# Performance work log

Measured on AMD Instinct MI355X. Metric: run time of the kernel, lower is better.

Reference implementation:

```python
import jax, jax.numpy as jnp
import numpy as np

BIG, SMALL = 13, 3
NK = 5                       # ceil(BIG / SMALL)
PADDING = SMALL - 1          # 2
EXTRA_PAD = PADDING - SMALL // 2   # 1
G = 2                        # group_in
C_OUT = 96
C_IN = G * C_OUT * NK        # 960
B, H, W = 16, 56, 56


def setup_inputs() -> dict:
    key = jax.random.key(0)
    k1, k2 = jax.random.split(key, 2)
    rng = np.random.default_rng(0)
    mid = BIG // 2
    real_pad = np.array([mid - i * SMALL - PADDING for i in range(NK)], dtype=np.int32)  # [4,1,-2,-5,-8]

    def perm_pads():
        # per output channel, a random permutation of the nk shift offsets
        return np.concatenate([rng.permutation(real_pad) for _ in range(C_OUT)])

    ph = np.stack([perm_pads() for _ in range(G)])  # (G, C_OUT*NK) horizontal shifts
    pv = np.stack([perm_pads() for _ in range(G)])  # (G, C_OUT*NK) vertical shifts
    pad_hv = np.concatenate([ph, pv], axis=0).T.astype(np.int32)  # (C_OUT*NK, 2*G)

    ids = []
    for _ in range(G):
        col = []
        for _ in range(C_OUT):
            arr = -np.ones(NK, dtype=np.int32)
            pos = rng.choice(NK, min(4, NK), replace=False)
            arr[pos] = np.arange(min(4, NK))
            col.append(arr)
        ids.append(np.concatenate(col))
    idx_identit = np.stack(ids).T.astype(np.int32)  # (C_OUT*NK, G)

    x = jax.random.normal(k1, (B, C_IN, H, W), jnp.float32)
    proj_w = jax.random.normal(k2, (C_OUT, C_IN), jnp.float32) * np.float32(1.0 / np.sqrt(C_IN))
    return {
        'x': x,
        'pad_hv': jnp.asarray(pad_hv),
        'idx_identit': jnp.asarray(idx_identit),
        'local_scale': jnp.ones((1, C_IN, 1, 1), jnp.float32),
        'local_bias': jnp.zeros((1, C_IN, 1, 1), jnp.float32),
        'proj_w': proj_w,
        'fuse_alpha': jnp.float32(0.7),
        'b': B, 'hout': H, 'wout': W,
    }


def reference(x, pad_hv, idx_identit, local_scale, local_bias, proj_w, fuse_alpha, b, hout, wout):
    p = EXTRA_PAD
    xp = jnp.pad(x, ((0, 0), (0, 0), (p, p), (p, p)), mode='edge')  # replicate pad
    Bx, Cin, Hp, Wp = xp.shape

    # per-channel shift offsets: channel ic = g*C_OUT*NK + slot, slot = co*NK + k
    ph = pad_hv[:, :G].T.reshape(-1)  # (C_IN,) horizontal (w-axis) shifts
    pv = pad_hv[:, G:].T.reshape(-1)  # (C_IN,) vertical (h-axis) shifts

    def gather_w(xc, s):  # xc: (B, Hp, Wp), s: scalar int shift
        idx = jnp.arange(wout) + p + s
        valid = ((idx >= 0) & (idx < Wp)).astype(xc.dtype)
        return xc[:, p:p + hout, jnp.clip(idx, 0, Wp - 1)] * valid[None, None, :]

    def gather_h(xc, s):
        idx = jnp.arange(hout) + p + s
        valid = ((idx >= 0) & (idx < Hp)).astype(xc.dtype)
        return xc[:, jnp.clip(idx, 0, Hp - 1), p:p + wout] * valid[None, :, None]

    xh = jax.vmap(gather_w, in_axes=(1, 0), out_axes=1)(xp, ph)  # (B, C_IN, hout, wout)
    xv = jax.vmap(gather_h, in_axes=(1, 0), out_axes=1)(xp, pv)
    x1 = xh.reshape(Bx, G, C_OUT, NK, hout, wout).sum((1, 3))    # horizontal-shift group
    x2 = xv.reshape(Bx, G, C_OUT, NK, hout, wout).sum((1, 3))    # vertical-shift group

    id_mask = (idx_identit.T.reshape(-1) >= 0).astype(xp.dtype)  # (C_IN,) identity slots
    x3 = (xp[:, :, p:p + hout, p:p + wout] * id_mask[None, :, None, None])
    x3 = x3.reshape(Bx, G, C_OUT, NK, hout, wout).sum((1, 3))    # identity group

    global_feat = (x1 + x2 + x3) / 3.0

    local = xp * (local_scale + 1e-5) + local_bias
    local = jax.image.resize(local, (Bx, Cin, hout, wout), method='bilinear')  # align_corners=False
    local = jnp.einsum('bchw,oc->bohw', local, proj_w)  # 1x1 conv, no bias

    return fuse_alpha * global_feat + (1.0 - fuse_alpha) * local
```

## Files before the change

### kernel.cpp

```cpp
#include <hip/hip_runtime.h>
#include <hip/hip_bf16.h>
#include <cstdint>
#include <cstddef>

#define B_    16
#define CIN   960
#define HH    56
#define WW_   56
#define GG    2
#define COUT  96
#define NK_   5
#define PIX   3136
#define NCH   30

#define WF_OFF   0
#define BIAS_OFF 46080
#define Y_OFF    46208

typedef __attribute__((ext_vector_type(8))) short bf16x8;
typedef __attribute__((ext_vector_type(4))) float f32x4;

__device__ __forceinline__ short f2b(float f) {
    union { float f; unsigned u; } c; c.f = f;
    unsigned r = (c.u + 0x7FFFu + ((c.u >> 16) & 1u)) >> 16;
    return (short)r;
}
__device__ __forceinline__ float b2f(short s) {
    union { unsigned u; float f; } c;
    c.u = ((unsigned)(unsigned short)s) << 16;
    return c.f;
}

#define GLOAD_LDS16(gp, lp)                                                        \
    __builtin_amdgcn_global_load_lds(                                              \
        (const __attribute__((address_space(1))) unsigned*)(gp),                   \
        (__attribute__((address_space(3))) unsigned*)(lp), 16, 0, 0)

#define WAITVM8() asm volatile("s_waitcnt vmcnt(8)" ::: "memory")
#define RBARRIER() asm volatile("s_barrier" ::: "memory")

__global__ void prep_wb(const float* __restrict__ pw, const float* __restrict__ sc,
                        short* __restrict__ wf) {
    int idx = blockIdx.x * 256 + threadIdx.x;
    if (idx >= NCH * 6 * 64) return;
    const int lane = idx & 63;
    const int nf   = idx >> 6;
    const int f    = nf % 6;
    const int n    = nf / 6;
    const int o    = f * 16 + (lane & 15);
    const int c0   = n * 32 + (lane >> 4) * 8;
    bf16x8 v;
#pragma unroll
    for (int k = 0; k < 8; ++k)
        v[k] = f2b(pw[o * CIN + c0 + k] * (sc[c0 + k] + 1e-5f));
    *(bf16x8*)(wf + (size_t)idx * 8) = v;
}

__global__ void prep_bias(const float* __restrict__ pw, const float* __restrict__ bi,
                          float* __restrict__ bias) {
    const int o = blockIdx.x;
    const int l = threadIdx.x;
    float s = 0.f;
    for (int c = l; c < CIN; c += 64) s += pw[o * CIN + c] * bi[c];
#pragma unroll
    for (int off = 32; off; off >>= 1) s += __shfl_down(s, off);
    if (l == 0) bias[o] = s;
}

__global__ __launch_bounds__(256)
void conv_mfma(const float* __restrict__ x, const short* __restrict__ wf,
               short* __restrict__ yb) {
    const int tid  = threadIdx.x;
    const int lane = tid & 63;
    const int wv   = tid >> 6;
    const int b    = blockIdx.y;
    const int px0  = blockIdx.x * 64;

    __shared__ __align__(16) char xs[3][8192];

    const float* xbase = x + (size_t)b * CIN * PIX + px0;

    const int pxl = wv * 16 + (lane & 15);
    const int kb  = lane >> 4;
    const int rbase = (pxl * 4) ^ (kb << 6);
    const short* const wfl = wf + lane * 8;

    f32x4 acc[6];
#pragma unroll
    for (int f = 0; f < 6; ++f) acc[f] = (f32x4){0.f, 0.f, 0.f, 0.f};

#define STAGE(bufp, c0)                                                          \
    {                                                                            \
        _Pragma("unroll")                                                        \
        for (int q = 0; q < 2; ++q) {                                            \
            const int i_  = wv * 2 + q;                                          \
            const int ch_ = (c0) + i_ * 4 + (lane >> 4);                         \
            const int px4 = (lane & 15) ^ (((i_ >> 1) & 3) << 2);                \
            GLOAD_LDS16(xbase + (size_t)ch_ * PIX + px4 * 4,                     \
                        (char*)(bufp) + i_ * 1024);                              \
        }                                                                        \
    }

#define WLOAD(dst, n2)                                                           \
    {                                                                            \
        _Pragma("unroll")                                                        \
        for (int f = 0; f < 6; ++f)                                              \
            dst[f] = *(const bf16x8*)(wfl + ((n2) * 6 + f) * 512);               \
    }

    bf16x8 afA[6], afB[6], afC[6];

    STAGE(xs[0], 0);
    STAGE(xs[1], 32);
    WLOAD(afA, 0);
    WLOAD(afB, 1);

#define STEP(n, BI, BS, CUR, NXT)                                                \
    {                                                                            \
        WAITVM8();                                                               \
        RBARRIER();                                                              \
        bf16x8 bfrag;                                                            \
        _Pragma("unroll")                                                        \
        for (int k = 0; k < 8; ++k)                                              \
            bfrag[k] = f2b(*(const float*)(xs[BI] + (kb * 8 + k) * 256 + rbase));\
        if ((n) + 2 < NCH) {                                                     \
            STAGE(xs[BS], ((n) + 2) * 32);                                       \
            WLOAD(NXT, (n) + 2);                                                 \
        }                                                                        \
        _Pragma("unroll")                                                        \
        for (int f = 0; f < 6; ++f)                                              \
            acc[f] = __builtin_amdgcn_mfma_f32_16x16x32_bf16(CUR[f], bfrag, acc[f], 0, 0, 0); \
    }

#pragma unroll 1
    for (int mm = 0; mm < 10; ++mm) {
        const int n0 = mm * 3;
        STEP(n0 + 0, 0, 2, afA, afC);
        STEP(n0 + 1, 1, 0, afB, afA);
        STEP(n0 + 2, 2, 1, afC, afB);
    }
#undef STEP
#undef WLOAD
#undef STAGE

    short* yp = yb + (size_t)b * COUT * PIX + px0 + pxl;
#pragma unroll
    for (int f = 0; f < 6; ++f) {
        const int o0 = f * 16 + (lane >> 4) * 4;
#pragma unroll
        for (int r = 0; r < 4; ++r)
            yp[(size_t)(o0 + r) * PIX] = f2b(acc[f][r]);
    }
}

__device__ __forceinline__ void rweights56(int o, short* idx, float* wt) {
    const float ratio = 58.0f / 56.0f;
    const float kinv  = 56.0f / 58.0f;
    const float sf = ((float)o + 0.5f) * ratio - 0.5f;
    const int f0 = (int)floorf(sf);
    float sum = 0.f;
#pragma unroll
    for (int t = 0; t < 4; ++t) {
        int i = f0 - 1 + t;
        float w = fmaxf(1.0f - fabsf(sf - (float)i) * kinv, 0.0f);
        if (i < 0 || i > 57) w = 0.0f;
        idx[t] = (short)min(HH - 1, max(0, i - 1));
        wt[t] = w;
        sum += w;
    }
    const float inv = 1.0f / sum;
#pragma unroll
    for (int t = 0; t < 4; ++t) wt[t] *= inv;
}

__global__ __launch_bounds__(256)
void finalize(const float* __restrict__ x, const int* __restrict__ pad_hv,
              const int* __restrict__ idt, const short* __restrict__ yb,
              const float* __restrict__ bias, const float* __restrict__ alpha_p,
              float* __restrict__ out) {
    const int bc = blockIdx.x;
    const int co = bc % COUT;
    const int b  = bc / COUT;
    const int t  = threadIdx.x;

    __shared__ float  ylds[PIX];
    __shared__ float4 wt4[56];
    __shared__ short4 id4[56];
    __shared__ int   ish[10], isv[10], ipl[10];
    __shared__ float fid[10];

    if (t < 10) {
        const int g = t / 5;
        const int k = t - g * 5;
        const int slot = co * NK_ + k;
        ish[t] = pad_hv[slot * 4 + g];
        isv[t] = pad_hv[slot * 4 + 2 + g];
        fid[t] = (idt[slot * 2 + g] >= 0) ? 1.f : 0.f;
        ipl[t] = (g * (COUT * NK_) + slot) * PIX;
    }
    if (t < 56) {
        short ii[4]; float ww[4];
        rweights56(t, ii, ww);
        wt4[t] = make_float4(ww[0], ww[1], ww[2], ww[3]);
        id4[t] = make_short4(ii[0], ii[1], ii[2], ii[3]);
    }
    {
        const short* yp = yb + (size_t)bc * PIX;
#pragma unroll 1
        for (int i = t; i < PIX / 4; i += 256) {
            const short4 s4 = *(const short4*)(yp + i * 4);
            *(float4*)(ylds + i * 4) =
                make_float4(b2f(s4.x), b2f(s4.y), b2f(s4.z), b2f(s4.w));
        }
    }
    __syncthreads();

    int   ish_r[10], isv_r[10], ipl_r[10];
    float fid_r[10];
#pragma unroll
    for (int p = 0; p < 10; ++p) {
        ish_r[p] = ish[p]; isv_r[p] = isv[p];
        ipl_r[p] = ipl[p]; fid_r[p] = fid[p];
    }

    const float alpha = alpha_p[0];
    const float ia    = 1.0f - alpha;
    const float bco   = bias[co];
    const float* xb = x + (size_t)b * CIN * PIX;
    float* op = out + (size_t)bc * PIX;

#pragma unroll 1
    for (int px = t; px < PIX; px += 256) {
        const int h = (px * 18725) >> 20;
        const int w = px - h * WW_;
        const int hrow = px - w;

        float accg = 0.f;
#pragma unroll
        for (int p = 0; p < 10; ++p) {
            const float* xc = xb + ipl_r[p];
            const int jw = w + ish_r[p];
            const float mh = (jw >= -1 && jw <= WW_) ? 1.f : 0.f;
            accg += mh * xc[hrow + min(WW_ - 1, max(0, jw))];

            const int iv = h + isv_r[p];
            const float mv = (iv >= -1 && iv <= HH) ? 1.f : 0.f;
            accg += mv * xc[min(HH - 1, max(0, iv)) * WW_ + w];

            accg += fid_r[p] * xc[px];
        }

        const float4 ww4 = wt4[w];
        const short4 iw4 = id4[w];
        const float4 wh4 = wt4[h];
        const short4 ih4 = id4[h];
        float accl = 0.f;
#pragma unroll
        for (int a = 0; a < 4; ++a) {
            const int row = ((const short*)&ih4)[a] * WW_;
            const float* yr = ylds + row;
            float rs;
            rs = ww4.x * yr[iw4.x];
            rs = fmaf(ww4.y, yr[iw4.y], rs);
            rs = fmaf(ww4.z, yr[iw4.z], rs);
            rs = fmaf(ww4.w, yr[iw4.w], rs);
            accl = fmaf(((const float*)&wh4)[a], rs, accl);
        }
        accl += bco;

        op[px] = alpha * accg * (1.0f / 3.0f) + ia * accl;
    }
}

extern "C" void kernel_launch(void* const* d_in, const int* in_sizes, int n_in,
                              void* d_out, int out_size, void* d_ws, size_t ws_size,
                              hipStream_t stream) {
    const float* x      = (const float*)d_in[0];
    const int*   pad_hv = (const int*)d_in[1];
    const int*   idt    = (const int*)d_in[2];
    const float* lsc    = (const float*)d_in[3];
    const float* lbi    = (const float*)d_in[4];
    const float* pw     = (const float*)d_in[5];
    const float* alpha  = (const float*)d_in[6];
    float* out = (float*)d_out;

    float* ws   = (float*)d_ws;
    short* wf   = (short*)(ws + WF_OFF);
    float* bias = ws + BIAS_OFF;
    short* yb   = (short*)(ws + Y_OFF);

    prep_wb<<<(NCH * 6 * 64 + 255) / 256, 256, 0, stream>>>(pw, lsc, wf);
    prep_bias<<<COUT, 64, 0, stream>>>(pw, lbi, bias);
    conv_mfma<<<dim3(PIX / 64, B_), 256, 0, stream>>>(x, wf, yb);
    finalize<<<B_ * COUT, 256, 0, stream>>>(x, pad_hv, idt, yb, bias, alpha, out);
}
```

Measured before the change: 100.5 us.

## Split conv GEMM across 8 waves and stage weights through LDS

The 1x1 projection GEMM now runs with 512 threads per block. The 8 waves are split 2x4 over output channels and pixels, so each wave keeps 3 MFMA accumulators instead of 6. Weight fragments are laid out per 32-channel chunk (8 KB) and copied into a triple-buffered LDS ring with global_load_lds, alongside the x tiles, instead of being loaded per wave into registers. This cuts register pressure and redundant global weight reads, at the cost of twice the LDS traffic and a bigger workspace offset. Each wave still converts its own x fragment to bf16.

```diff
diff --git a/kernel.cpp b/kernel.cpp
--- a/kernel.cpp
+++ b/kernel.cpp
@@ -14,8 +14,8 @@
 #define NCH   30
 
 #define WF_OFF   0
-#define BIAS_OFF 46080
-#define Y_OFF    46208
+#define BIAS_OFF 61440
+#define Y_OFF    61568
 
 typedef __attribute__((ext_vector_type(8))) short bf16x8;
 typedef __attribute__((ext_vector_type(4))) float f32x4;
@@ -35,9 +35,6 @@
     __builtin_amdgcn_global_load_lds(                                              \
         (const __attribute__((address_space(1))) unsigned*)(gp),                   \
         (__attribute__((address_space(3))) unsigned*)(lp), 16, 0, 0)
-
-#define WAITVM8() asm volatile("s_waitcnt vmcnt(8)" ::: "memory")
-#define RBARRIER() asm volatile("s_barrier" ::: "memory")
 
 __global__ void prep_wb(const float* __restrict__ pw, const float* __restrict__ sc,
                         short* __restrict__ wf) {
@@ -53,7 +50,7 @@
 #pragma unroll
     for (int k = 0; k < 8; ++k)
         v[k] = f2b(pw[o * CIN + c0 + k] * (sc[c0 + k] + 1e-5f));
-    *(bf16x8*)(wf + (size_t)idx * 8) = v;
+    *(bf16x8*)((char*)wf + (size_t)n * 8192 + (f * 64 + lane) * 16) = v;
 }
 
 __global__ void prep_bias(const float* __restrict__ pw, const float* __restrict__ bi,
@@ -67,90 +64,87 @@
     if (l == 0) bias[o] = s;
 }
 
-__global__ __launch_bounds__(256)
+__global__ __launch_bounds__(512)
 void conv_mfma(const float* __restrict__ x, const short* __restrict__ wf,
                short* __restrict__ yb) {
     const int tid  = threadIdx.x;
     const int lane = tid & 63;
     const int wv   = tid >> 6;
+    const int m    = wv >> 2;
+    const int n    = wv & 3;
     const int b    = blockIdx.y;
     const int px0  = blockIdx.x * 64;
 
-    __shared__ __align__(16) char xs[3][8192];
+    __shared__ __align__(16) char xsb[3 * 8192];
+    __shared__ __align__(16) char wlb[3 * 8192];
 
     const float* xbase = x + (size_t)b * CIN * PIX + px0;
-
-    const int pxl = wv * 16 + (lane & 15);
-    const int kb  = lane >> 4;
-    const int rbase = (pxl * 4) ^ (kb << 6);
-    const short* const wfl = wf + lane * 8;
-
-    f32x4 acc[6];
-#pragma unroll
-    for (int f = 0; f < 6; ++f) acc[f] = (f32x4){0.f, 0.f, 0.f, 0.f};
-
-#define STAGE(bufp, c0)                                                          \
+    const char*  wfB   = (const char*)wf;
+
+    const int sch  = wv * 4 + (lane >> 4);
+    const int sS   = (wv >> 1) & 3;
+    const int soff = (((lane >> 2) & 3) ^ sS) * 16 + (lane & 3) * 4;
+    const int wsub = wv * 1024 + lane * 16;
+
+    const int kb    = lane >> 4;
+    const int bcol  = (lane & 15) * 4;
+    const int bslot = ((n ^ kb) & 3) * 64;
+    const int babs  = kb * 2048 + bslot + bcol;
+    const int abase = m * 3072 + lane * 16;
+
+    f32x4 acc0 = {0.f, 0.f, 0.f, 0.f};
+    f32x4 acc1 = {0.f, 0.f, 0.f, 0.f};
+    f32x4 acc2 = {0.f, 0.f, 0.f, 0.f};
+
+#define STAGE(BS, c0)                                                            \
     {                                                                            \
-        _Pragma("unroll")                                                        \
-        for (int q = 0; q < 2; ++q) {                                            \
-            const int i_  = wv * 2 + q;                                          \
-            const int ch_ = (c0) + i_ * 4 + (lane >> 4);                         \
-            const int px4 = (lane & 15) ^ (((i_ >> 1) & 3) << 2);                \
-            GLOAD_LDS16(xbase + (size_t)ch_ * PIX + px4 * 4,                     \
-                        (char*)(bufp) + i_ * 1024);                              \
-        }                                                                        \
-    }
-
-#define WLOAD(dst, n2)                                                           \
+        GLOAD_LDS16(xbase + (size_t)((c0) + sch) * PIX + soff,                   \
+                    xsb + (BS) * 8192 + wv * 1024);                              \
+        GLOAD_LDS16(wfB + (size_t)((c0) >> 5) * 8192 + wsub,                     \
+                    wlb + (BS) * 8192 + wv * 1024);                              \
+    }
+
+    STAGE(0, 0);
+    STAGE(1, 32);
+
+#define STEP(n_, BI, BS, VM)                                                     \
     {                                                                            \
-        _Pragma("unroll")                                                        \
-        for (int f = 0; f < 6; ++f)                                              \
-            dst[f] = *(const bf16x8*)(wfl + ((n2) * 6 + f) * 512);               \
-    }
-
-    bf16x8 afA[6], afB[6], afC[6];
-
-    STAGE(xs[0], 0);
-    STAGE(xs[1], 32);
-    WLOAD(afA, 0);
-    WLOAD(afB, 1);
-
-#define STEP(n, BI, BS, CUR, NXT)                                                \
-    {                                                                            \
-        WAITVM8();                                                               \
-        RBARRIER();                                                              \
+        asm volatile("s_waitcnt vmcnt(" #VM ")" ::: "memory");                   \
+        asm volatile("s_barrier" ::: "memory");                                  \
         bf16x8 bfrag;                                                            \
         _Pragma("unroll")                                                        \
         for (int k = 0; k < 8; ++k)                                              \
-            bfrag[k] = f2b(*(const float*)(xs[BI] + (kb * 8 + k) * 256 + rbase));\
-        if ((n) + 2 < NCH) {                                                     \
-            STAGE(xs[BS], ((n) + 2) * 32);                                       \
-            WLOAD(NXT, (n) + 2);                                                 \
-        }                                                                        \
-        _Pragma("unroll")                                                        \
-        for (int f = 0; f < 6; ++f)                                              \
-            acc[f] = __builtin_amdgcn_mfma_f32_16x16x32_bf16(CUR[f], bfrag, acc[f], 0, 0, 0); \
+            bfrag[k] = f2b(*(const float*)(xsb + (BI) * 8192 + babs + k * 256)); \
+        const bf16x8 af0 = *(const bf16x8*)(wlb + (BI) * 8192 + abase);          \
+        const bf16x8 af1 = *(const bf16x8*)(wlb + (BI) * 8192 + abase + 1024);   \
+        const bf16x8 af2 = *(const bf16x8*)(wlb + (BI) * 8192 + abase + 2048);   \
+        if ((n_) + 2 < NCH) STAGE(BS, ((n_) + 2) * 32);                          \
+        acc0 = __builtin_amdgcn_mfma_f32_16x16x32_bf16(af0, bfrag, acc0, 0,0,0); \
+        acc1 = __builtin_amdgcn_mfma_f32_16x16x32_bf16(af1, bfrag, acc1, 0,0,0); \
+        acc2 = __builtin_amdgcn_mfma_f32_16x16x32_bf16(af2, bfrag, acc2, 0,0,0); \
     }
 
 #pragma unroll 1
-    for (int mm = 0; mm < 10; ++mm) {
+    for (int mm = 0; mm < 9; ++mm) {
         const int n0 = mm * 3;
-        STEP(n0 + 0, 0, 2, afA, afC);
-        STEP(n0 + 1, 1, 0, afB, afA);
-        STEP(n0 + 2, 2, 1, afC, afB);
-    }
+        STEP(n0 + 0, 0, 2, 2);
+        STEP(n0 + 1, 1, 0, 2);
+        STEP(n0 + 2, 2, 1, 2);
+    }
+    STEP(27, 0, 2, 2);
+    STEP(28, 1, 0, 2);
+    STEP(29, 2, 1, 0);
 #undef STEP
-#undef WLOAD
 #undef STAGE
 
-    short* yp = yb + (size_t)b * COUT * PIX + px0 + pxl;
-#pragma unroll
-    for (int f = 0; f < 6; ++f) {
-        const int o0 = f * 16 + (lane >> 4) * 4;
-#pragma unroll
-        for (int r = 0; r < 4; ++r)
-            yp[(size_t)(o0 + r) * PIX] = f2b(acc[f][r]);
-    }
+    short* yp = yb + (size_t)b * COUT * PIX + px0 + n * 16 + (lane & 15);
+    const int o0 = m * 48 + (lane >> 4) * 4;
+#pragma unroll
+    for (int r = 0; r < 4; ++r) yp[(size_t)(o0 +      r) * PIX] = f2b(acc0[r]);
+#pragma unroll
+    for (int r = 0; r < 4; ++r) yp[(size_t)(o0 + 16 + r) * PIX] = f2b(acc1[r]);
+#pragma unroll
+    for (int r = 0; r < 4; ++r) yp[(size_t)(o0 + 32 + r) * PIX] = f2b(acc2[r]);
 }
 
 __device__ __forceinline__ void rweights56(int o, short* idx, float* wt) {
@@ -291,6 +285,6 @@
 
     prep_wb<<<(NCH * 6 * 64 + 255) / 256, 256, 0, stream>>>(pw, lsc, wf);
     prep_bias<<<COUT, 64, 0, stream>>>(pw, lbi, bias);
-    conv_mfma<<<dim3(PIX / 64, B_), 256, 0, stream>>>(x, wf, yb);
+    conv_mfma<<<dim3(PIX / 64, B_), 512, 0, stream>>>(x, wf, yb);
     finalize<<<B_ * COUT, 256, 0, stream>>>(x, pad_hv, idt, yb, bias, alpha, out);
 }
```

Measured after the change: 93.50 us. -7.0%, faster.
